# Optimization experiments

Measured on AMD Instinct MI355X. Metric: run time of the kernel, lower is better.

Reference implementation:

```python
import jax, jax.numpy as jnp
import numpy as np

B, NH, T, D = 2, 16, 2048, 64

def setup_inputs() -> dict:
    key = jax.random.key(0)
    kq, kk, kv = jax.random.split(key, 3)
    Q = jax.random.normal(kq, (B, NH, T, D), dtype=jnp.float32)
    K = jax.random.normal(kk, (B, NH, T, D), dtype=jnp.float32)
    V = jax.random.normal(kv, (B, NH, T, D), dtype=jnp.float32)
    return {"Q": Q, "K": K, "V": V}

def reference(Q, K, V):
    # scores: [B, nh, T, T]
    Dh = Q.shape[-1]
    scale = 1.0 / jnp.sqrt(jnp.asarray(Dh, Q.dtype))
    scores = jnp.einsum('bhtd,bhsd->bhts', Q, K) * scale
    Tq = Q.shape[2]
    causal = jnp.tril(jnp.ones((Tq, Tq), dtype=bool))
    scores = jnp.where(causal, scores, jnp.asarray(-jnp.inf, scores.dtype))
    attn = jax.nn.softmax(scores, axis=-1)
    return jnp.einsum('bhts,bhsd->bhtd', attn, V)
```

## Files before the change

### kernel.cpp

```cpp
#include <hip/hip_runtime.h>
#include <hip/hip_bf16.h>


typedef __bf16 bf16;
typedef __bf16 bf16x4 __attribute__((ext_vector_type(4)));
typedef __bf16 bf16x8 __attribute__((ext_vector_type(8)));
typedef float floatx4 __attribute__((ext_vector_type(4)));

#define T_SEQ 2048
#define DH 64
#define TKS 32
#define BHN 32
#define CEXP 0.18033688011112042f

__device__ __forceinline__ void gload16(const bf16* g, bf16* l) {
    __builtin_amdgcn_global_load_lds(
        (const __attribute__((address_space(1))) void*)g,
        (__attribute__((address_space(3))) void*)l, 16, 0, 0);
}

__global__ __launch_bounds__(256) void prep(const float* __restrict__ K,
                                            const float* __restrict__ V,
                                            bf16* __restrict__ Kb,
                                            bf16* __restrict__ Vt) {
    const int bid = (int)blockIdx.x;
    const int tid = (int)threadIdx.x;
    if (bid < 512) {
        size_t i = ((size_t)bid * 256 + tid) * 8;
        #pragma unroll
        for (int it = 0; it < 4; ++it) {
            float4 a = *(const float4*)(K + i + 0);
            float4 b = *(const float4*)(K + i + 4);
            bf16x8 o;
            o[0]=(bf16)a.x; o[1]=(bf16)a.y; o[2]=(bf16)a.z; o[3]=(bf16)a.w;
            o[4]=(bf16)b.x; o[5]=(bf16)b.y; o[6]=(bf16)b.z; o[7]=(bf16)b.w;
            *(bf16x8*)(Kb + i) = o;
            i += (size_t)512 * 256 * 8;
        }
        return;
    }
    __shared__ bf16 tile[2][64][72];
    const int vb = bid - 512;
    const int bh = vb & (BHN - 1);
    const int tp = (vb >> 5) * 128;
    #pragma unroll
    for (int tt = 0; tt < 2; ++tt) {
        const int r = tid >> 2;
        const int c = (tid & 3) * 16;
        const float* s = V + ((size_t)bh * T_SEQ + tp + tt * 64 + r) * DH + c;
        float4 f0 = *(const float4*)(s + 0);
        float4 f1 = *(const float4*)(s + 4);
        float4 f2 = *(const float4*)(s + 8);
        float4 f3 = *(const float4*)(s + 12);
        bf16x8 p0, p1;
        p0[0]=(bf16)f0.x; p0[1]=(bf16)f0.y; p0[2]=(bf16)f0.z; p0[3]=(bf16)f0.w;
        p0[4]=(bf16)f1.x; p0[5]=(bf16)f1.y; p0[6]=(bf16)f1.z; p0[7]=(bf16)f1.w;
        p1[0]=(bf16)f2.x; p1[1]=(bf16)f2.y; p1[2]=(bf16)f2.z; p1[3]=(bf16)f2.w;
        p1[4]=(bf16)f3.x; p1[5]=(bf16)f3.y; p1[6]=(bf16)f3.z; p1[7]=(bf16)f3.w;
        *(bf16x8*)&tile[tt][r][c + 0] = p0;
        *(bf16x8*)&tile[tt][r][c + 8] = p1;
    }
    __syncthreads();
    #pragma unroll
    for (int tt = 0; tt < 2; ++tt) {
        const int d   = tid >> 2;
        const int tch = (tid & 3) * 16;
        bf16x8 o0, o1;
        #pragma unroll
        for (int j = 0; j < 8; ++j) { o0[j] = tile[tt][tch + j][d]; o1[j] = tile[tt][tch + 8 + j][d]; }
        bf16* o = Vt + ((size_t)bh * DH + d) * T_SEQ + tp + tt * 64 + tch;
        *(bf16x8*)(o + 0) = o0;
        *(bf16x8*)(o + 8) = o1;
    }
}

__global__ __launch_bounds__(256, 2)
void fa_fwd(const float* __restrict__ Qg, const bf16* __restrict__ Kb,
            const bf16* __restrict__ Vt, float* __restrict__ Og)
{
    __shared__ __align__(16) bf16 smem[32768];

    const int gid = (int)blockIdx.x;
    const int bh  = gid & (BHN - 1);
    const int m   = gid >> 5;
    const int B   = 64 - 2 * m;
    const int qh  = (31 - m) * 64;
    const int ql  = m * 64;

    const int tid  = (int)threadIdx.x;
    const int wave = tid >> 6;
    const int lane = tid & 63;
    const int quad = lane >> 4;
    const int l16  = lane & 15;

    const int tw0 = (wave < 2) ? wave * 17 : 34 + (wave - 2) * 16;
    const int tw1 = tw0 + ((wave < 2) ? 17 : 16);

    bf16* W   = smem + wave * 8192;
    bf16* Kb0 = W;
    bf16* Kb1 = W + 2048;
    bf16* Vb  = W + 4096;
    bf16* Pw  = W + 6144;

    const bf16* Kbh = Kb + (size_t)bh * (T_SEQ * DH);
    const bf16* Vbh = Vt + (size_t)bh * (DH * T_SEQ);
    const size_t qrb = (size_t)bh * T_SEQ;

    const int rl  = lane >> 3;
    const int kch = (lane & 7) ^ (rl & 7);
    const int vr  = lane >> 2;
    const int vch = (lane & 3) ^ ((lane >> 3) & 3);
    const int psw = (l16 >> 1) & 3;

    bool heavyNow = (tw0 < B);
    int  qbase    = heavyNow ? qh : ql;

    bf16x8 qb[4][2];
    auto loadQ = [&](int qb0) {
        #pragma unroll
        for (int nt = 0; nt < 4; ++nt) {
            const int qrow = qb0 + nt * 16 + l16;
            #pragma unroll
            for (int kk = 0; kk < 2; ++kk) {
                const float* s = Qg + (qrb + qrow) * DH + kk * 32 + quad * 8;
                float4 f0 = *(const float4*)(s);
                float4 f1 = *(const float4*)(s + 4);
                bf16x8 t;
                t[0]=(bf16)f0.x; t[1]=(bf16)f0.y; t[2]=(bf16)f0.z; t[3]=(bf16)f0.w;
                t[4]=(bf16)f1.x; t[5]=(bf16)f1.y; t[6]=(bf16)f1.z; t[7]=(bf16)f1.w;
                qb[nt][kk] = t;
            }
        }
    };
    loadQ(qbase);

    floatx4 oacc[4][4];
    #pragma unroll
    for (int mt = 0; mt < 4; ++mt)
        #pragma unroll
        for (int nt = 0; nt < 4; ++nt) oacc[mt][nt] = (floatx4){0.f,0.f,0.f,0.f};
    float lpart[4] = {0.f, 0.f, 0.f, 0.f};
    bf16x4 parked[16];
    #pragma unroll
    for (int f = 0; f < 16; ++f) parked[f] = (bf16x4){(bf16)0.f,(bf16)0.f,(bf16)0.f,(bf16)0.f};
    float lpark[4] = {0.f, 0.f, 0.f, 0.f};
    bool hasPark = false;

    auto kTileOf = [&](int t) { return (t < B) ? t : (t - B); };

    auto stageK = [&](int kt, bf16* dst) {
        const bf16* kg = Kbh + (size_t)kt * TKS * DH;
        #pragma unroll
        for (int g = 0; g < 4; ++g)
            gload16(kg + (size_t)(g * 8 + rl) * DH + kch * 8, dst + g * 512);
    };
    auto stageV = [&](int kt) {
        const bf16* vg = Vbh + kt * TKS;
        #pragma unroll
        for (int g = 0; g < 4; ++g)
            gload16(vg + (size_t)(g * 16 + vr) * T_SEQ + vch * 8, Vb + g * 512);
    };

    stageK(kTileOf(tw0), Kb0);

    for (int t = tw0; t < tw1; ++t) {
        if (heavyNow && t == B) {
            #pragma unroll
            for (int f = 0; f < 16; ++f) {
                bf16x4 w;
                #pragma unroll
                for (int e = 0; e < 4; ++e) w[e] = (bf16)oacc[f >> 2][f & 3][e];
                parked[f] = w;
            }
            #pragma unroll
            for (int nt = 0; nt < 4; ++nt) { lpark[nt] = lpart[nt]; lpart[nt] = 0.f; }
            #pragma unroll
            for (int mt = 0; mt < 4; ++mt)
                #pragma unroll
                for (int nt = 0; nt < 4; ++nt) oacc[mt][nt] = (floatx4){0.f,0.f,0.f,0.f};
            hasPark = true;
            heavyNow = false;
            qbase = ql;
            loadQ(ql);
        }

        const int cur = (t - tw0) & 1;
        bf16* Kcur = cur ? Kb1 : Kb0;
        const int kt = kTileOf(t);
        const int k0 = kt * TKS;

        stageV(kt);
        stageK(kTileOf(t + 1), cur ? Kb0 : Kb1);
        __builtin_amdgcn_s_waitcnt(0x0F78);

        #pragma unroll
        for (int mt = 0; mt < 2; ++mt) {
            floatx4 sa[4];
            #pragma unroll
            for (int nt = 0; nt < 4; ++nt) sa[nt] = (floatx4){0.f,0.f,0.f,0.f};
            #pragma unroll
            for (int kk = 0; kk < 2; ++kk) {
                bf16x8 kf = *(const bf16x8*)&Kcur[(mt * 16 + l16) * 64 + (((kk * 4 + quad) ^ (l16 & 7)) * 8)];
                #pragma unroll
                for (int nt = 0; nt < 4; ++nt)
                    sa[nt] = __builtin_amdgcn_mfma_f32_16x16x32_bf16(kf, qb[nt][kk], sa[nt], 0, 0, 0);
            }
            if (k0 + TKS - 1 > qbase) {
                #pragma unroll
                for (int nt = 0; nt < 4; ++nt) {
                    const int qg = qbase + nt * 16 + l16;
                    #pragma unroll
                    for (int r = 0; r < 4; ++r) {
                        const int keyg = k0 + mt * 16 + quad * 4 + r;
                        if (keyg > qg) sa[nt][r] = -INFINITY;
                    }
                }
            }
            #pragma unroll
            for (int nt = 0; nt < 4; ++nt) {
                bf16x4 w;
                #pragma unroll
                for (int r = 0; r < 4; ++r) {
                    const float pv = __builtin_amdgcn_exp2f(CEXP * sa[nt][r]);
                    lpart[nt] += pv;
                    w[r] = (bf16)pv;
                }
                const int slot = (mt * 2 + (quad >> 1)) ^ psw;
                *(bf16x4*)&Pw[(nt * 16 + l16) * 32 + slot * 8 + (quad & 1) * 4] = w;
            }
        }

        bf16x8 pf[4];
        #pragma unroll
        for (int nt = 0; nt < 4; ++nt)
            pf[nt] = *(const bf16x8*)&Pw[(nt * 16 + l16) * 32 + ((quad ^ psw) * 8)];

        __builtin_amdgcn_s_waitcnt(0x0F74);

        #pragma unroll
        for (int mt = 0; mt < 4; ++mt) {
            bf16x8 vf = *(const bf16x8*)&Vb[(mt * 16 + l16) * 32 + ((quad ^ psw) * 8)];
            #pragma unroll
            for (int nt = 0; nt < 4; ++nt)
                oacc[mt][nt] = __builtin_amdgcn_mfma_f32_16x16x32_bf16(vf, pf[nt], oacc[mt][nt], 0, 0, 0);
        }
    }

    __syncthreads();
    const bool hH = (tw0 < B);
    const bool hL = (tw1 > B);
    if (wave >= 1 && hH) {
        bf16* a = smem + (wave - 1) * 4608;
        float* al = (float*)(a + 4096);
        #pragma unroll
        for (int f = 0; f < 16; ++f) {
            bf16x4 w;
            if (hasPark) w = parked[f];
            else {
                #pragma unroll
                for (int e = 0; e < 4; ++e) w[e] = (bf16)oacc[f >> 2][f & 3][e];
            }
            *(bf16x4*)&a[(f * 64 + lane) * 4] = w;
        }
        #pragma unroll
        for (int nt = 0; nt < 4; ++nt)
            al[nt * 64 + lane] = hasPark ? lpark[nt] : lpart[nt];
    }
    if (wave >= 2 && hL) {
        bf16* a = smem + (wave + 1) * 4608;
        float* al = (float*)(a + 4096);
        #pragma unroll
        for (int f = 0; f < 16; ++f) {
            bf16x4 w;
            #pragma unroll
            for (int e = 0; e < 4; ++e) w[e] = (bf16)oacc[f >> 2][f & 3][e];
            *(bf16x4*)&a[(f * 64 + lane) * 4] = w;
        }
        #pragma unroll
        for (int nt = 0; nt < 4; ++nt)
            al[nt * 64 + lane] = lpart[nt];
    }
    __syncthreads();

    if (wave <= 1) {
        int qfin;
        if (wave == 0) {
            qfin = qh;
            const int nA = (B > 50) ? 3 : ((B > 34) ? 2 : 1);
            for (int i = 0; i < nA; ++i) {
                const bf16* a = smem + i * 4608;
                const float* al = (const float*)(a + 4096);
                #pragma unroll
                for (int f = 0; f < 16; ++f) {
                    bf16x4 w = *(const bf16x4*)&a[(f * 64 + lane) * 4];
                    #pragma unroll
                    for (int e = 0; e < 4; ++e) oacc[f >> 2][f & 3][e] += (float)w[e];
                }
                #pragma unroll
                for (int nt = 0; nt < 4; ++nt) lpart[nt] += al[nt * 64 + lane];
            }
        } else {
            qfin = ql;
            #pragma unroll
            for (int mt = 0; mt < 4; ++mt)
                #pragma unroll
                for (int nt = 0; nt < 4; ++nt) oacc[mt][nt] = (floatx4){0.f,0.f,0.f,0.f};
            #pragma unroll
            for (int nt = 0; nt < 4; ++nt) lpart[nt] = 0.f;
            const int i0 = (B < 50) ? 3 : 4;
            for (int i = i0; i <= 4; ++i) {
                const bf16* a = smem + i * 4608;
                const float* al = (const float*)(a + 4096);
                #pragma unroll
                for (int f = 0; f < 16; ++f) {
                    bf16x4 w = *(const bf16x4*)&a[(f * 64 + lane) * 4];
                    #pragma unroll
                    for (int e = 0; e < 4; ++e) oacc[f >> 2][f & 3][e] += (float)w[e];
                }
                #pragma unroll
                for (int nt = 0; nt < 4; ++nt) lpart[nt] += al[nt * 64 + lane];
            }
        }
        float invl[4];
        #pragma unroll
        for (int nt = 0; nt < 4; ++nt) {
            float v = lpart[nt];
            v += __shfl_xor(v, 16);
            v += __shfl_xor(v, 32);
            invl[nt] = 1.0f / v;
        }
        #pragma unroll
        for (int nt = 0; nt < 4; ++nt) {
            const size_t qrow = qrb + qfin + nt * 16 + l16;
            #pragma unroll
            for (int mt = 0; mt < 4; ++mt) {
                float4 o;
                o.x = oacc[mt][nt][0] * invl[nt];
                o.y = oacc[mt][nt][1] * invl[nt];
                o.z = oacc[mt][nt][2] * invl[nt];
                o.w = oacc[mt][nt][3] * invl[nt];
                *(float4*)&Og[qrow * DH + mt * 16 + quad * 4] = o;
            }
        }
    }
}

extern "C" void kernel_launch(void* const* d_in, const int* in_sizes, int n_in,
                              void* d_out, int out_size, void* d_ws, size_t ws_size,
                              hipStream_t stream) {
    const float* Q = (const float*)d_in[0];
    const float* K = (const float*)d_in[1];
    const float* V = (const float*)d_in[2];
    float* O = (float*)d_out;
    (void)in_sizes; (void)n_in; (void)out_size; (void)ws_size;

    const size_t nelem = (size_t)BHN * T_SEQ * DH;
    bf16* Kbf = (bf16*)d_ws;
    bf16* Vtb = Kbf + nelem;

    prep<<<dim3(1024), dim3(256), 0, stream>>>(K, V, Kbf, Vtb);
    fa_fwd<<<dim3(512), dim3(256), 0, stream>>>(Q, Kbf, Vtb, O);
}
```

Baseline: 124.0 us.

## Load K/V fragments directly into registers with double-buffering, park partials in LDS

Replaces the per-wave LDS staging of K and V tiles (global_load_lds plus waitcnt) with direct global-to-register loads of MFMA fragments, double-buffered across iterations through ping-pong register arrays and a two-step unrolled loop. The heavy-row partial accumulator is now written straight to the shared reduction area when the wave switches query blocks, instead of being kept in registers, which frees VGPRs. LDS use drops to only the P buffer and the reduction area. The cost is more register pressure from the prefetched fragments, less coalesced global reads for the fragment layout, and possible LDS aliasing between the parked region and the P buffers.

```diff
diff --git a/kernel.cpp b/kernel.cpp
--- a/kernel.cpp
+++ b/kernel.cpp
@@ -12,12 +12,6 @@
 #define TKS 32
 #define BHN 32
 #define CEXP 0.18033688011112042f
-
-__device__ __forceinline__ void gload16(const bf16* g, bf16* l) {
-    __builtin_amdgcn_global_load_lds(
-        (const __attribute__((address_space(1))) void*)g,
-        (__attribute__((address_space(3))) void*)l, 16, 0, 0);
-}
 
 __global__ __launch_bounds__(256) void prep(const float* __restrict__ K,
                                             const float* __restrict__ V,
@@ -78,7 +72,7 @@
 void fa_fwd(const float* __restrict__ Qg, const bf16* __restrict__ Kb,
             const bf16* __restrict__ Vt, float* __restrict__ Og)
 {
-    __shared__ __align__(16) bf16 smem[32768];
+    __shared__ __align__(16) bf16 smem[31232];
 
     const int gid = (int)blockIdx.x;
     const int bh  = gid & (BHN - 1);
@@ -92,28 +86,20 @@
     const int lane = tid & 63;
     const int quad = lane >> 4;
     const int l16  = lane & 15;
+    const int psw  = (l16 >> 1) & 3;
 
     const int tw0 = (wave < 2) ? wave * 17 : 34 + (wave - 2) * 16;
     const int tw1 = tw0 + ((wave < 2) ? 17 : 16);
 
-    bf16* W   = smem + wave * 8192;
-    bf16* Kb0 = W;
-    bf16* Kb1 = W + 2048;
-    bf16* Vb  = W + 4096;
-    bf16* Pw  = W + 6144;
+    bf16* Pw = smem + 23040 + wave * 2048;
 
     const bf16* Kbh = Kb + (size_t)bh * (T_SEQ * DH);
     const bf16* Vbh = Vt + (size_t)bh * (DH * T_SEQ);
     const size_t qrb = (size_t)bh * T_SEQ;
 
-    const int rl  = lane >> 3;
-    const int kch = (lane & 7) ^ (rl & 7);
-    const int vr  = lane >> 2;
-    const int vch = (lane & 3) ^ ((lane >> 3) & 3);
-    const int psw = (l16 >> 1) & 3;
-
     bool heavyNow = (tw0 < B);
     int  qbase    = heavyNow ? qh : ql;
+    bool hasPark  = false;
 
     bf16x8 qb[4][2];
     auto loadQ = [&](int qb0) {
@@ -140,59 +126,51 @@
         #pragma unroll
         for (int nt = 0; nt < 4; ++nt) oacc[mt][nt] = (floatx4){0.f,0.f,0.f,0.f};
     float lpart[4] = {0.f, 0.f, 0.f, 0.f};
-    bf16x4 parked[16];
-    #pragma unroll
-    for (int f = 0; f < 16; ++f) parked[f] = (bf16x4){(bf16)0.f,(bf16)0.f,(bf16)0.f,(bf16)0.f};
-    float lpark[4] = {0.f, 0.f, 0.f, 0.f};
-    bool hasPark = false;
-
-    auto kTileOf = [&](int t) { return (t < B) ? t : (t - B); };
-
-    auto stageK = [&](int kt, bf16* dst) {
-        const bf16* kg = Kbh + (size_t)kt * TKS * DH;
-        #pragma unroll
-        for (int g = 0; g < 4; ++g)
-            gload16(kg + (size_t)(g * 8 + rl) * DH + kch * 8, dst + g * 512);
+
+    auto loadKV = [&](int kt, bf16x8 (&kf)[4], bf16x8 (&vf)[4]) {
+        const int k0 = kt * TKS;
+        #pragma unroll
+        for (int mt = 0; mt < 2; ++mt)
+            #pragma unroll
+            for (int kk = 0; kk < 2; ++kk)
+                kf[mt * 2 + kk] = *(const bf16x8*)(Kbh + (size_t)(k0 + mt * 16 + l16) * DH + kk * 32 + quad * 8);
+        #pragma unroll
+        for (int mt = 0; mt < 4; ++mt)
+            vf[mt] = *(const bf16x8*)(Vbh + (size_t)(mt * 16 + l16) * T_SEQ + k0 + quad * 8);
     };
-    auto stageV = [&](int kt) {
-        const bf16* vg = Vbh + kt * TKS;
-        #pragma unroll
-        for (int g = 0; g < 4; ++g)
-            gload16(vg + (size_t)(g * 16 + vr) * T_SEQ + vch * 8, Vb + g * 512);
+
+    auto parkHeavy = [&]() {
+        bf16* a = smem + (wave - 1) * 4608;
+        float* al = (float*)(a + 4096);
+        #pragma unroll
+        for (int f = 0; f < 16; ++f) {
+            bf16x4 w;
+            #pragma unroll
+            for (int e = 0; e < 4; ++e) w[e] = (bf16)oacc[f >> 2][f & 3][e];
+            *(bf16x4*)&a[(f * 64 + lane) * 4] = w;
+        }
+        #pragma unroll
+        for (int nt = 0; nt < 4; ++nt) { al[nt * 64 + lane] = lpart[nt]; lpart[nt] = 0.f; }
+        #pragma unroll
+        for (int mt = 0; mt < 4; ++mt)
+            #pragma unroll
+            for (int nt = 0; nt < 4; ++nt) oacc[mt][nt] = (floatx4){0.f,0.f,0.f,0.f};
+        hasPark = true;
+        heavyNow = false;
+        qbase = ql;
+        loadQ(ql);
     };
 
-    stageK(kTileOf(tw0), Kb0);
-
-    for (int t = tw0; t < tw1; ++t) {
-        if (heavyNow && t == B) {
-            #pragma unroll
-            for (int f = 0; f < 16; ++f) {
-                bf16x4 w;
-                #pragma unroll
-                for (int e = 0; e < 4; ++e) w[e] = (bf16)oacc[f >> 2][f & 3][e];
-                parked[f] = w;
-            }
-            #pragma unroll
-            for (int nt = 0; nt < 4; ++nt) { lpark[nt] = lpart[nt]; lpart[nt] = 0.f; }
-            #pragma unroll
-            for (int mt = 0; mt < 4; ++mt)
-                #pragma unroll
-                for (int nt = 0; nt < 4; ++nt) oacc[mt][nt] = (floatx4){0.f,0.f,0.f,0.f};
-            hasPark = true;
-            heavyNow = false;
-            qbase = ql;
-            loadQ(ql);
-        }
-
-        const int cur = (t - tw0) & 1;
-        bf16* Kcur = cur ? Kb1 : Kb0;
-        const int kt = kTileOf(t);
+    auto body = [&](int t, bf16x8 (&kc)[4], bf16x8 (&vc)[4],
+                    bf16x8 (&kn)[4], bf16x8 (&vn)[4]) {
+        if (heavyNow && t == B) parkHeavy();
+        const int kt = (t < B) ? t : t - B;
         const int k0 = kt * TKS;
-
-        stageV(kt);
-        stageK(kTileOf(t + 1), cur ? Kb0 : Kb1);
-        __builtin_amdgcn_s_waitcnt(0x0F78);
-
+        const int tn = t + 1;
+        if (tn < tw1) {
+            const int ktn = (tn < B) ? tn : tn - B;
+            loadKV(ktn, kn, vn);
+        }
         #pragma unroll
         for (int mt = 0; mt < 2; ++mt) {
             floatx4 sa[4];
@@ -200,7 +178,7 @@
             for (int nt = 0; nt < 4; ++nt) sa[nt] = (floatx4){0.f,0.f,0.f,0.f};
             #pragma unroll
             for (int kk = 0; kk < 2; ++kk) {
-                bf16x8 kf = *(const bf16x8*)&Kcur[(mt * 16 + l16) * 64 + (((kk * 4 + quad) ^ (l16 & 7)) * 8)];
+                bf16x8 kf = kc[mt * 2 + kk];
                 #pragma unroll
                 for (int nt = 0; nt < 4; ++nt)
                     sa[nt] = __builtin_amdgcn_mfma_f32_16x16x32_bf16(kf, qb[nt][kk], sa[nt], 0, 0, 0);
@@ -229,42 +207,45 @@
                 *(bf16x4*)&Pw[(nt * 16 + l16) * 32 + slot * 8 + (quad & 1) * 4] = w;
             }
         }
-
         bf16x8 pf[4];
         #pragma unroll
         for (int nt = 0; nt < 4; ++nt)
             pf[nt] = *(const bf16x8*)&Pw[(nt * 16 + l16) * 32 + ((quad ^ psw) * 8)];
-
-        __builtin_amdgcn_s_waitcnt(0x0F74);
-
         #pragma unroll
         for (int mt = 0; mt < 4; ++mt) {
-            bf16x8 vf = *(const bf16x8*)&Vb[(mt * 16 + l16) * 32 + ((quad ^ psw) * 8)];
             #pragma unroll
             for (int nt = 0; nt < 4; ++nt)
-                oacc[mt][nt] = __builtin_amdgcn_mfma_f32_16x16x32_bf16(vf, pf[nt], oacc[mt][nt], 0, 0, 0);
-        }
+                oacc[mt][nt] = __builtin_amdgcn_mfma_f32_16x16x32_bf16(vc[mt], pf[nt], oacc[mt][nt], 0, 0, 0);
+        }
+    };
+
+    bf16x8 kA[4], vA[4], kB[4], vB[4];
+    loadKV((tw0 < B) ? tw0 : tw0 - B, kA, vA);
+
+    int t = tw0;
+    while (true) {
+        body(t, kA, vA, kB, vB);
+        if (++t == tw1) break;
+        body(t, kB, vB, kA, vA);
+        if (++t == tw1) break;
     }
 
     __syncthreads();
     const bool hH = (tw0 < B);
     const bool hL = (tw1 > B);
-    if (wave >= 1 && hH) {
+    if (wave >= 1 && hH && !hasPark) {
         bf16* a = smem + (wave - 1) * 4608;
         float* al = (float*)(a + 4096);
         #pragma unroll
         for (int f = 0; f < 16; ++f) {
             bf16x4 w;
-            if (hasPark) w = parked[f];
-            else {
-                #pragma unroll
-                for (int e = 0; e < 4; ++e) w[e] = (bf16)oacc[f >> 2][f & 3][e];
-            }
+            #pragma unroll
+            for (int e = 0; e < 4; ++e) w[e] = (bf16)oacc[f >> 2][f & 3][e];
             *(bf16x4*)&a[(f * 64 + lane) * 4] = w;
         }
         #pragma unroll
         for (int nt = 0; nt < 4; ++nt)
-            al[nt * 64 + lane] = hasPark ? lpark[nt] : lpart[nt];
+            al[nt * 64 + lane] = lpart[nt];
     }
     if (wave >= 2 && hL) {
         bf16* a = smem + (wave + 1) * 4608;
```

After: 132.6 us. 1.07x slower.

## Double-buffer V tiles alongside K and reuse K buffer for P

Applied to the files above, without the earlier changes.

V tiles are now double-buffered and prefetched one iteration ahead together with K, so the V load no longer has to finish inside the same iteration that issues it. The P staging area now reuses the current K buffer, which is free once the QK MFMAs have read it. The QK loop is also reordered so both row tiles of scores are computed before masking and exponentiation, giving more independent MFMAs in flight. The cost is more accumulator registers and reliance on the K reads completing before P overwrites that buffer within the wave.

```diff
diff --git a/kernel.cpp b/kernel.cpp
--- a/kernel.cpp
+++ b/kernel.cpp
@@ -92,15 +92,12 @@
     const int lane = tid & 63;
     const int quad = lane >> 4;
     const int l16  = lane & 15;
+    const int psw  = (l16 >> 1) & 3;
 
     const int tw0 = (wave < 2) ? wave * 17 : 34 + (wave - 2) * 16;
     const int tw1 = tw0 + ((wave < 2) ? 17 : 16);
 
-    bf16* W   = smem + wave * 8192;
-    bf16* Kb0 = W;
-    bf16* Kb1 = W + 2048;
-    bf16* Vb  = W + 4096;
-    bf16* Pw  = W + 6144;
+    bf16* W = smem + wave * 8192;
 
     const bf16* Kbh = Kb + (size_t)bh * (T_SEQ * DH);
     const bf16* Vbh = Vt + (size_t)bh * (DH * T_SEQ);
@@ -110,10 +107,10 @@
     const int kch = (lane & 7) ^ (rl & 7);
     const int vr  = lane >> 2;
     const int vch = (lane & 3) ^ ((lane >> 3) & 3);
-    const int psw = (l16 >> 1) & 3;
 
     bool heavyNow = (tw0 < B);
     int  qbase    = heavyNow ? qh : ql;
+    bool hasPark  = false;
 
     bf16x8 qb[4][2];
     auto loadQ = [&](int qb0) {
@@ -144,7 +141,6 @@
     #pragma unroll
     for (int f = 0; f < 16; ++f) parked[f] = (bf16x4){(bf16)0.f,(bf16)0.f,(bf16)0.f,(bf16)0.f};
     float lpark[4] = {0.f, 0.f, 0.f, 0.f};
-    bool hasPark = false;
 
     auto kTileOf = [&](int t) { return (t < B) ? t : (t - B); };
 
@@ -154,14 +150,15 @@
         for (int g = 0; g < 4; ++g)
             gload16(kg + (size_t)(g * 8 + rl) * DH + kch * 8, dst + g * 512);
     };
-    auto stageV = [&](int kt) {
+    auto stageV = [&](int kt, bf16* dst) {
         const bf16* vg = Vbh + kt * TKS;
         #pragma unroll
         for (int g = 0; g < 4; ++g)
-            gload16(vg + (size_t)(g * 16 + vr) * T_SEQ + vch * 8, Vb + g * 512);
+            gload16(vg + (size_t)(g * 16 + vr) * T_SEQ + vch * 8, dst + g * 512);
     };
 
-    stageK(kTileOf(tw0), Kb0);
+    stageK(kTileOf(tw0), W);
+    stageV(kTileOf(tw0), W + 4096);
 
     for (int t = tw0; t < tw1; ++t) {
         if (heavyNow && t == B) {
@@ -185,64 +182,74 @@
         }
 
         const int cur = (t - tw0) & 1;
-        bf16* Kcur = cur ? Kb1 : Kb0;
+        bf16* Kcur = W + cur * 2048;
+        bf16* Vcur = W + 4096 + cur * 2048;
+        bf16* Pw   = Kcur;
         const int kt = kTileOf(t);
         const int k0 = kt * TKS;
 
-        stageV(kt);
-        stageK(kTileOf(t + 1), cur ? Kb0 : Kb1);
-        __builtin_amdgcn_s_waitcnt(0x0F78);
-
-        #pragma unroll
-        for (int mt = 0; mt < 2; ++mt) {
-            floatx4 sa[4];
-            #pragma unroll
-            for (int nt = 0; nt < 4; ++nt) sa[nt] = (floatx4){0.f,0.f,0.f,0.f};
-            #pragma unroll
-            for (int kk = 0; kk < 2; ++kk) {
+        const bool pf = (t + 1 < tw1);
+        if (pf) {
+            const int ktn = kTileOf(t + 1);
+            stageK(ktn, W + (cur ^ 1) * 2048);
+            stageV(ktn, W + 4096 + (cur ^ 1) * 2048);
+            __builtin_amdgcn_s_waitcnt(0x0F78);
+        } else {
+            __builtin_amdgcn_s_waitcnt(0x0F70);
+        }
+
+        floatx4 sa[2][4];
+        #pragma unroll
+        for (int mt = 0; mt < 2; ++mt)
+            #pragma unroll
+            for (int nt = 0; nt < 4; ++nt) sa[mt][nt] = (floatx4){0.f,0.f,0.f,0.f};
+        #pragma unroll
+        for (int kk = 0; kk < 2; ++kk) {
+            #pragma unroll
+            for (int mt = 0; mt < 2; ++mt) {
                 bf16x8 kf = *(const bf16x8*)&Kcur[(mt * 16 + l16) * 64 + (((kk * 4 + quad) ^ (l16 & 7)) * 8)];
                 #pragma unroll
                 for (int nt = 0; nt < 4; ++nt)
-                    sa[nt] = __builtin_amdgcn_mfma_f32_16x16x32_bf16(kf, qb[nt][kk], sa[nt], 0, 0, 0);
-            }
-            if (k0 + TKS - 1 > qbase) {
+                    sa[mt][nt] = __builtin_amdgcn_mfma_f32_16x16x32_bf16(kf, qb[nt][kk], sa[mt][nt], 0, 0, 0);
+            }
+        }
+        if (k0 + TKS - 1 > qbase) {
+            #pragma unroll
+            for (int mt = 0; mt < 2; ++mt)
                 #pragma unroll
                 for (int nt = 0; nt < 4; ++nt) {
                     const int qg = qbase + nt * 16 + l16;
                     #pragma unroll
                     for (int r = 0; r < 4; ++r) {
                         const int keyg = k0 + mt * 16 + quad * 4 + r;
-                        if (keyg > qg) sa[nt][r] = -INFINITY;
+                        if (keyg > qg) sa[mt][nt][r] = -INFINITY;
                     }
                 }
-            }
+        }
+        #pragma unroll
+        for (int mt = 0; mt < 2; ++mt)
             #pragma unroll
             for (int nt = 0; nt < 4; ++nt) {
                 bf16x4 w;
                 #pragma unroll
                 for (int r = 0; r < 4; ++r) {
-                    const float pv = __builtin_amdgcn_exp2f(CEXP * sa[nt][r]);
+                    const float pv = __builtin_amdgcn_exp2f(CEXP * sa[mt][nt][r]);
                     lpart[nt] += pv;
                     w[r] = (bf16)pv;
                 }
                 const int slot = (mt * 2 + (quad >> 1)) ^ psw;
                 *(bf16x4*)&Pw[(nt * 16 + l16) * 32 + slot * 8 + (quad & 1) * 4] = w;
             }
-        }
-
-        bf16x8 pf[4];
+        bf16x8 pfr[4];
         #pragma unroll
         for (int nt = 0; nt < 4; ++nt)
-            pf[nt] = *(const bf16x8*)&Pw[(nt * 16 + l16) * 32 + ((quad ^ psw) * 8)];
-
-        __builtin_amdgcn_s_waitcnt(0x0F74);
-
+            pfr[nt] = *(const bf16x8*)&Pw[(nt * 16 + l16) * 32 + ((quad ^ psw) * 8)];
         #pragma unroll
         for (int mt = 0; mt < 4; ++mt) {
-            bf16x8 vf = *(const bf16x8*)&Vb[(mt * 16 + l16) * 32 + ((quad ^ psw) * 8)];
+            bf16x8 vf = *(const bf16x8*)&Vcur[(mt * 16 + l16) * 32 + ((quad ^ psw) * 8)];
             #pragma unroll
             for (int nt = 0; nt < 4; ++nt)
-                oacc[mt][nt] = __builtin_amdgcn_mfma_f32_16x16x32_bf16(vf, pf[nt], oacc[mt][nt], 0, 0, 0);
+                oacc[mt][nt] = __builtin_amdgcn_mfma_f32_16x16x32_bf16(vf, pfr[nt], oacc[mt][nt], 0, 0, 0);
         }
     }
 
```

Result: no change. 122.4 us (-1.3%).
